# Kernel optimization log

Measured on AMD Instinct MI355X. Metric: run time of the kernel, lower is better.

## Reference

```python
import jax, jax.numpy as jnp
import numpy as np

N = 50000      # nodes
E = 640000     # edges
F_IN = 128
F_OUT = 128


def setup_inputs() -> dict:
    key = jax.random.key(0)
    k1, k2, k3, k4, k5 = jax.random.split(key, 5)
    x = jax.random.normal(k1, (N, F_IN), jnp.float32)
    # binary observation mask (torch: mask.float())
    mask = (jax.random.uniform(k2, (N, F_IN)) < 0.5).astype(jnp.float32)
    edge_index = jax.random.randint(k3, (2, E), 0, N, dtype=jnp.int32)
    W = jax.random.normal(k4, (F_OUT, F_IN), jnp.float32) / np.sqrt(F_IN)
    b = jax.random.normal(k5, (F_OUT,), jnp.float32) * 0.01
    return {"x": x, "mask": mask, "edge_index": edge_index, "W": W, "b": b}


def reference(x, mask, edge_index, W, b):
    row, col = edge_index[0], edge_index[1]

    # --- get_symmetrically_normalized_adjacency: DAD = D^-1/2 A D^-1/2 ---
    ones_e = jnp.ones((edge_index.shape[1],), x.dtype)
    deg = jax.ops.segment_sum(ones_e, col, num_segments=N)
    dinv = jnp.where(deg > 0, deg ** -0.5, 0.0)  # inf -> 0
    w = dinv[row] * dinv[col]                    # [E] normalized edge weights

    def spmm(m):  # (adj @ m)[i] = sum_{e: row_e=i} w_e * m[col_e]
        return jax.ops.segment_sum(w[:, None] * m[col], row, num_segments=N)

    # x[x.isnan()] = 0
    x = jnp.nan_to_num(x)

    # adj @ ones_like(x) == rowsum(adj) broadcast over features
    rowsum = jax.ops.segment_sum(w, row, num_segments=N)  # [N]
    numerator = rowsum[:, None] * spmm(mask * x)          # [N, F_IN]
    denominator = spmm(mask)                              # [N, F_IN]
    ratio = jnp.nan_to_num(numerator / denominator)

    return ratio @ W.T + b
```

## Files before the change

kernel.cpp:

```cpp
#include <hip/hip_runtime.h>
#include <math.h>

#define NN 50000
#define NE 640000
#define F  128
#define NB 196
#define PACKB 12500
#define CHB 256
#define ECHUNK 2500
#define WPAD 136
#define SRCW_N (NE + 8 * NN)

typedef __attribute__((ext_vector_type(8))) short short8;
typedef __attribute__((ext_vector_type(4))) float floatx4;

__device__ inline unsigned f2bf_pk(float f0, float f1) {
    unsigned u0 = __float_as_uint(f0), u1 = __float_as_uint(f1);
    u0 = (u0 + 0x7fffu + ((u0 >> 16) & 1u)) >> 16;
    u1 = (u1 + 0x7fffu + ((u1 >> 16) & 1u)) >> 16;
    return (u1 << 16) | u0;
}

__device__ inline unsigned ilv4(unsigned a, unsigned b) {
    a = (a | (a << 2)) & 0x33u; a = (a | (a << 1)) & 0x55u;
    b = (b | (b << 2)) & 0x33u; b = (b | (b << 1)) & 0x55u;
    return a | (b << 1);
}

__global__ __launch_bounds__(256) void pc_kernel(const float* __restrict__ x,
                                                 const float* __restrict__ mask,
                                                 const int* __restrict__ row,
                                                 const int* __restrict__ col,
                                                 unsigned* __restrict__ mx,
                                                 unsigned char* __restrict__ rec,
                                                 int* __restrict__ crow,
                                                 int* __restrict__ ccol) {
    if (blockIdx.x < PACKB) {
        int lane = threadIdx.x & 63;
        int n = blockIdx.x * 4 + (threadIdx.x >> 6);
        float2 xv = ((const float2*)x)[(size_t)n * 64 + lane];
        float2 mv = ((const float2*)mask)[(size_t)n * 64 + lane];
        float x0 = (xv.x != xv.x) ? 0.f : xv.x;
        float x1 = (xv.y != xv.y) ? 0.f : xv.y;
        float p0 = (mv.x != 0.f) ? x0 : 0.f;
        float p1 = (mv.y != 0.f) ? x1 : 0.f;
        mx[(size_t)n * 64 + lane] = f2bf_pk(p0, p1);
        unsigned long long b0 = __ballot(mv.x != 0.f);
        unsigned long long b1 = __ballot(mv.y != 0.f);
        if (lane < 16) {
            unsigned nib0 = (unsigned)(b0 >> (4 * lane)) & 0xFu;
            unsigned nib1 = (unsigned)(b1 >> (4 * lane)) & 0xFu;
            rec[(size_t)n * 16 + lane] = (unsigned char)ilv4(nib0, nib1);
        }
    } else {
        __shared__ int hr[NB], hc[NB];
        for (int i = threadIdx.x; i < NB; i += 256) { hr[i] = 0; hc[i] = 0; }
        __syncthreads();
        int bid = blockIdx.x - PACKB;
        int e0 = bid * ECHUNK, e1 = e0 + ECHUNK;
        for (int e = e0 + threadIdx.x; e < e1; e += 256) {
            atomicAdd(&hr[row[e] >> 8], 1);
            atomicAdd(&hc[col[e] >> 8], 1);
        }
        __syncthreads();
        for (int i = threadIdx.x; i < NB; i += 256) {
            atomicAdd(&crow[i], hr[i]);
            atomicAdd(&ccol[i], hc[i]);
        }
    }
}

__global__ __launch_bounds__(256) void cscan_kernel(const int* __restrict__ crow,
                                                    const int* __restrict__ ccol,
                                                    int* __restrict__ crow_base,
                                                    int* __restrict__ ccol_base,
                                                    int* __restrict__ crow_cur,
                                                    int* __restrict__ ccol_cur,
                                                    int* __restrict__ rowstart_p) {
    __shared__ int ws[4];
    int t = threadIdx.x, lane = t & 63, wid = t >> 6;
    {
        int v = (t < NB) ? crow[t] : 0;
        int incl = v;
        #pragma unroll
        for (int off = 1; off < 64; off <<= 1) { int s = __shfl_up(incl, off); if (lane >= off) incl += s; }
        if (lane == 63) ws[wid] = incl;
        __syncthreads();
        int wbase = 0;
        for (int k = 0; k < wid; k++) wbase += ws[k];
        int ex = wbase + incl - v;
        if (t < NB) { crow_base[t] = ex; crow_cur[t] = ex; }
        if (t == 0) { crow_base[NB] = NE; rowstart_p[NN] = NE + 8 * NN; }
        __syncthreads();
    }
    {
        int v = (t < NB) ? ccol[t] : 0;
        int incl = v;
        #pragma unroll
        for (int off = 1; off < 64; off <<= 1) { int s = __shfl_up(incl, off); if (lane >= off) incl += s; }
        if (lane == 63) ws[wid] = incl;
        __syncthreads();
        int wbase = 0;
        for (int k = 0; k < wid; k++) wbase += ws[k];
        int ex = wbase + incl - v;
        if (t < NB) { ccol_base[t] = ex; ccol_cur[t] = ex; }
        if (t == 0) ccol_base[NB] = NE;
    }
}

__global__ __launch_bounds__(256) void scatter_kernel(const int* __restrict__ row,
                                                      const int* __restrict__ col,
                                                      int* __restrict__ crow_cur,
                                                      int* __restrict__ ccol_cur,
                                                      unsigned* __restrict__ rrec,
                                                      unsigned char* __restrict__ crec) {
    __shared__ int cntR[NB], cntC[NB], curR[NB], curC[NB];
    for (int i = threadIdx.x; i < NB; i += 256) { cntR[i] = 0; cntC[i] = 0; }
    __syncthreads();
    int e0 = blockIdx.x * ECHUNK, e1 = e0 + ECHUNK;
    for (int e = e0 + threadIdx.x; e < e1; e += 256) {
        atomicAdd(&cntR[row[e] >> 8], 1);
        atomicAdd(&cntC[col[e] >> 8], 1);
    }
    __syncthreads();
    for (int i = threadIdx.x; i < NB; i += 256) {
        curR[i] = atomicAdd(&crow_cur[i], cntR[i]);
        curC[i] = atomicAdd(&ccol_cur[i], cntC[i]);
    }
    __syncthreads();
    for (int e = e0 + threadIdx.x; e < e1; e += 256) {
        int r = row[e], c = col[e];
        int pr = atomicAdd(&curR[r >> 8], 1);
        rrec[pr] = ((unsigned)(r & 255) << 16) | (unsigned)c;
        int pc = atomicAdd(&curC[c >> 8], 1);
        crec[pc] = (unsigned char)(c & 255);
    }
}

__global__ __launch_bounds__(256) void finecol_kernel(const unsigned char* __restrict__ crec,
                                                      const int* __restrict__ ccol_base,
                                                      float* __restrict__ dinv) {
    __shared__ int hist[256];
    int b = blockIdx.x;
    int s0 = ccol_base[b], s1 = ccol_base[b + 1];
    int t = threadIdx.x;
    hist[t] = 0;
    __syncthreads();
    for (int j = s0 + t; j < s1; j += 256)
        atomicAdd(&hist[crec[j]], 1);
    __syncthreads();
    int node = b * 256 + t;
    if (node < NN) {
        int d = hist[t];
        dinv[node] = (d > 0) ? rsqrtf((float)d) : 0.0f;
    }
}

__global__ __launch_bounds__(256) void finerow_kernel(const unsigned* __restrict__ rrec,
                                                      const int* __restrict__ crow_base,
                                                      const float* __restrict__ dinv,
                                                      int* __restrict__ rowstart_p,
                                                      unsigned* __restrict__ srcs_w) {
    __shared__ int hist[256];
    __shared__ int ws[4];
    int b = blockIdx.x;
    int s0 = crow_base[b], s1 = crow_base[b + 1];
    int t = threadIdx.x, lane = t & 63, wid = t >> 6;
    hist[t] = 0;
    __syncthreads();
    for (int j = s0 + t; j < s1; j += 256)
        atomicAdd(&hist[(rrec[j] >> 16) & 255], 1);
    __syncthreads();
    int v = hist[t];
    int incl = v;
    #pragma unroll
    for (int off = 1; off < 64; off <<= 1) { int s = __shfl_up(incl, off); if (lane >= off) incl += s; }
    if (lane == 63) ws[wid] = incl;
    __syncthreads();
    int wbase = 0;
    for (int k = 0; k < wid; k++) wbase += ws[k];
    int ex = wbase + incl - v;
    int pbase = s0 + 2048 * b;
    int node = b * 256 + t;
    if (node < NN) rowstart_p[node] = pbase + ex + 8 * t;
    hist[t] = ex + 8 * t;
    __syncthreads();
    for (int j = s0 + t; j < s1; j += 256) {
        unsigned r2 = rrec[j];
        int c = r2 & 0xFFFF;
        int pos = atomicAdd(&hist[(r2 >> 16) & 255], 1);
        srcs_w[pbase + pos] = f2bf_pk(0.f, dinv[c]) | (unsigned)c;
    }
}

__global__ __launch_bounds__(256) void gather_kernel(
        const int* __restrict__ rowstart_p, const unsigned* __restrict__ srcs_w,
        const float* __restrict__ dinv,
        const uint4* __restrict__ mxv, const unsigned char* __restrict__ rec,
        unsigned* __restrict__ rb) {
    int lane = threadIdx.x & 63;
    int r = blockIdx.x * 4 + (threadIdx.x >> 6);
    int l16 = lane & 15, sub = lane >> 4;
    int s0p = rowstart_p[r];
    int L = rowstart_p[r + 1] - s0p - 8;
    float dr = dinv[r];
    floatx4 n0 = (floatx4)(0.f), n1 = (floatx4)(0.f);
    floatx4 d0 = (floatx4)(0.f), d1 = (floatx4)(0.f);
    float S = 0.f;

    for (int j = 0; j < L; j += 8) {
        #pragma unroll
        for (int g = 0; g < 2; g++) {
            unsigned u = srcs_w[s0p + j + 4 * g + sub];
            int c = u & 0xFFFFu;
            float w = __uint_as_float(u & 0xFFFF0000u);
            uint4 m4 = mxv[c * 16 + l16];
            unsigned mb = rec[c * 16 + l16];
            floatx4 fa, fb;
            fa.x = __uint_as_float(m4.x << 16); fa.y = __uint_as_float(m4.x & 0xffff0000u);
            fa.z = __uint_as_float(m4.y << 16); fa.w = __uint_as_float(m4.y & 0xffff0000u);
            fb.x = __uint_as_float(m4.z << 16); fb.y = __uint_as_float(m4.z & 0xffff0000u);
            fb.z = __uint_as_float(m4.w << 16); fb.w = __uint_as_float(m4.w & 0xffff0000u);
            n0 += w * fa;
            n1 += w * fb;
            d0.x += ((mb >> 0) & 1u) ? w : 0.f;
            d0.y += ((mb >> 1) & 1u) ? w : 0.f;
            d0.z += ((mb >> 2) & 1u) ? w : 0.f;
            d0.w += ((mb >> 3) & 1u) ? w : 0.f;
            d1.x += ((mb >> 4) & 1u) ? w : 0.f;
            d1.y += ((mb >> 5) & 1u) ? w : 0.f;
            d1.z += ((mb >> 6) & 1u) ? w : 0.f;
            d1.w += ((mb >> 7) & 1u) ? w : 0.f;
            S += w;
        }
    }

    float num[8] = {n0.x, n0.y, n0.z, n0.w, n1.x, n1.y, n1.z, n1.w};
    float den[8] = {d0.x, d0.y, d0.z, d0.w, d1.x, d1.y, d1.z, d1.w};
    #pragma unroll
    for (int q = 0; q < 8; q++) {
        num[q] += __shfl_xor(num[q], 16); num[q] += __shfl_xor(num[q], 32);
        den[q] += __shfl_xor(den[q], 16); den[q] += __shfl_xor(den[q], 32);
    }
    S += __shfl_xor(S, 16); S += __shfl_xor(S, 32);

    if (sub == 0) {
        float kf = dr * S;
        float o[8];
        #pragma unroll
        for (int q = 0; q < 8; q++)
            o[q] = (den[q] != 0.f) ? kf * num[q] * __builtin_amdgcn_rcpf(den[q]) : 0.f;
        uint4 pk;
        pk.x = f2bf_pk(o[0], o[1]);
        pk.y = f2bf_pk(o[2], o[3]);
        pk.z = f2bf_pk(o[4], o[5]);
        pk.w = f2bf_pk(o[6], o[7]);
        ((uint4*)rb)[(size_t)r * 16 + l16] = pk;
    }
}

__global__ __launch_bounds__(256) void gemm_kernel(const unsigned short* __restrict__ Ab,
                                                   const float* __restrict__ W,
                                                   const float* __restrict__ bias,
                                                   float* __restrict__ out) {
    __shared__ unsigned short Wlds[F * WPAD];
    int tid = threadIdx.x;

    for (int i = tid * 4; i < F * F; i += 256 * 4) {
        int c = i >> 7, k = i & 127;
        float4 v = *(const float4*)(W + i);
        unsigned lo = f2bf_pk(v.x, v.y);
        unsigned hi = f2bf_pk(v.z, v.w);
        *(uint2*)&Wlds[c * WPAD + k] = make_uint2(lo, hi);
    }
    __syncthreads();

    int lane = tid & 63, wid = tid >> 6;
    int m = lane & 15, quad = lane >> 4;
    int arow = blockIdx.x * 64 + wid * 16 + m;
    int lrow = (arow < NN) ? arow : (NN - 1);
    const unsigned short* Arow = Ab + (size_t)lrow * F + quad * 8;

    floatx4 acc[8];
    #pragma unroll
    for (int nt = 0; nt < 8; nt++) acc[nt] = (floatx4)(0.f);

    #pragma unroll
    for (int step = 0; step < 4; step++) {
        short8 af = *(const short8*)(Arow + step * 32);
        #pragma unroll
        for (int nt = 0; nt < 8; nt++) {
            short8 bf = *(const short8*)&Wlds[(nt * 16 + m) * WPAD + step * 32 + quad * 8];
            acc[nt] = __builtin_amdgcn_mfma_f32_16x16x32_bf16(af, bf, acc[nt], 0, 0, 0);
        }
    }

    int orow0 = blockIdx.x * 64 + wid * 16 + quad * 4;
    #pragma unroll
    for (int nt = 0; nt < 8; nt++) {
        float bv = bias[nt * 16 + m];
        #pragma unroll
        for (int p = 0; p < 4; p++) {
            int gr = orow0 + p;
            if (gr < NN) out[(size_t)gr * F + nt * 16 + m] = acc[nt][p] + bv;
        }
    }
}

extern "C" void kernel_launch(void* const* d_in, const int* in_sizes, int n_in,
                              void* d_out, int out_size, void* d_ws, size_t ws_size,
                              hipStream_t stream) {
    const float* x    = (const float*)d_in[0];
    const float* mask = (const float*)d_in[1];
    const int*   ei   = (const int*)d_in[2];
    const float* W    = (const float*)d_in[3];
    const float* b    = (const float*)d_in[4];
    float* out = (float*)d_out;

    const int* row = ei;
    const int* col = ei + NE;

    unsigned*       mx        = (unsigned*)d_ws;
    unsigned*       rb        = mx + (size_t)NN * 64;
    unsigned*       srcs_w    = rb + (size_t)NN * 64;
    unsigned*       rrec      = srcs_w + SRCW_N;
    unsigned char*  rec       = (unsigned char*)(rrec + NE);
    unsigned char*  crec      = rec + (size_t)NN * 16;
    float*          dinv      = (float*)(crec + NE);
    int*            crow      = (int*)(dinv + NN);
    int*            ccol      = crow + NB;
    int*            crow_base = ccol + NB;
    int*            ccol_base = crow_base + NB + 1;
    int*            crow_cur  = ccol_base + NB + 1;
    int*            ccol_cur  = crow_cur + NB;
    int*            rowstart_p= ccol_cur + NB;

    hipMemsetAsync(crow, 0, 2 * NB * sizeof(int), stream);
    hipMemsetAsync(srcs_w, 0, (size_t)SRCW_N * sizeof(unsigned), stream);

    pc_kernel<<<PACKB + CHB, 256, 0, stream>>>(x, mask, row, col, mx, rec, crow, ccol);
    cscan_kernel<<<1, 256, 0, stream>>>(crow, ccol, crow_base, ccol_base,
                                        crow_cur, ccol_cur, rowstart_p);
    scatter_kernel<<<CHB, 256, 0, stream>>>(row, col, crow_cur, ccol_cur, rrec, crec);
    finecol_kernel<<<NB, 256, 0, stream>>>(crec, ccol_base, dinv);
    finerow_kernel<<<NB, 256, 0, stream>>>(rrec, crow_base, dinv, rowstart_p, srcs_w);
    gather_kernel<<<NN / 4, 256, 0, stream>>>(rowstart_p, srcs_w, dinv,
                                              (const uint4*)mx, rec, rb);
    gemm_kernel<<<(NN + 63) / 64, 256, 0, stream>>>((const unsigned short*)rb, W, b, out);
}
```

Measured before the change: 202.6 us.

## Merge fine row/col kernels, store 16-bit sources and fold dinv into mask records

Merges the degree-histogram and row-bucketing kernels into one launch, so the row side no longer waits for dinv and writes plain 16-bit column indices instead of packed index+weight words. Column dinv now lives inside each node's 32-byte mask record, so the gather reads weight and mask bits from one line. Padding slots point to a zeroed dummy node, which removes the large memset of the source array. It also switches to a true divide in the ratio and nontemporal stores in the GEMM output, at the cost of a slightly larger per-node record.

```diff
diff --git a/kernel.cpp b/kernel.cpp
--- a/kernel.cpp
+++ b/kernel.cpp
@@ -9,7 +9,8 @@
 #define CHB 256
 #define ECHUNK 2500
 #define WPAD 136
-#define SRCW_N (NE + 8 * NN)
+#define RPAD 8
+#define SRCS_N (NE + 256 * RPAD * NB)
 
 typedef __attribute__((ext_vector_type(8))) short short8;
 typedef __attribute__((ext_vector_type(4))) float floatx4;
@@ -50,7 +51,7 @@
         if (lane < 16) {
             unsigned nib0 = (unsigned)(b0 >> (4 * lane)) & 0xFu;
             unsigned nib1 = (unsigned)(b1 >> (4 * lane)) & 0xFu;
-            rec[(size_t)n * 16 + lane] = (unsigned char)ilv4(nib0, nib1);
+            rec[(size_t)n * 32 + lane] = (unsigned char)ilv4(nib0, nib1);
         }
     } else {
         __shared__ int hr[NB], hc[NB];
@@ -76,9 +77,13 @@
                                                     int* __restrict__ ccol_base,
                                                     int* __restrict__ crow_cur,
                                                     int* __restrict__ ccol_cur,
-                                                    int* __restrict__ rowstart_p) {
+                                                    int* __restrict__ rowstart_p,
+                                                    unsigned* __restrict__ mx,
+                                                    unsigned char* __restrict__ rec) {
     __shared__ int ws[4];
     int t = threadIdx.x, lane = t & 63, wid = t >> 6;
+    if (t < 64) mx[(size_t)NN * 64 + t] = 0u;
+    if (t < 8)  ((unsigned*)(rec + (size_t)NN * 32))[t] = 0u;
     {
         int v = (t < NB) ? crow[t] : 0;
         int incl = v;
@@ -90,7 +95,7 @@
         for (int k = 0; k < wid; k++) wbase += ws[k];
         int ex = wbase + incl - v;
         if (t < NB) { crow_base[t] = ex; crow_cur[t] = ex; }
-        if (t == 0) { crow_base[NB] = NE; rowstart_p[NN] = NE + 8 * NN; }
+        if (t == 0) { crow_base[NB] = NE; rowstart_p[NN] = NE + RPAD * NN; }
         __syncthreads();
     }
     {
@@ -137,73 +142,71 @@
     }
 }
 
-__global__ __launch_bounds__(256) void finecol_kernel(const unsigned char* __restrict__ crec,
-                                                      const int* __restrict__ ccol_base,
-                                                      float* __restrict__ dinv) {
-    __shared__ int hist[256];
-    int b = blockIdx.x;
-    int s0 = ccol_base[b], s1 = ccol_base[b + 1];
-    int t = threadIdx.x;
-    hist[t] = 0;
-    __syncthreads();
-    for (int j = s0 + t; j < s1; j += 256)
-        atomicAdd(&hist[crec[j]], 1);
-    __syncthreads();
-    int node = b * 256 + t;
-    if (node < NN) {
-        int d = hist[t];
-        dinv[node] = (d > 0) ? rsqrtf((float)d) : 0.0f;
-    }
-}
-
-__global__ __launch_bounds__(256) void finerow_kernel(const unsigned* __restrict__ rrec,
-                                                      const int* __restrict__ crow_base,
-                                                      const float* __restrict__ dinv,
-                                                      int* __restrict__ rowstart_p,
-                                                      unsigned* __restrict__ srcs_w) {
+__global__ __launch_bounds__(256) void fine_kernel(const unsigned* __restrict__ rrec,
+                                                   const unsigned char* __restrict__ crec,
+                                                   const int* __restrict__ crow_base,
+                                                   const int* __restrict__ ccol_base,
+                                                   int* __restrict__ rowstart_p,
+                                                   unsigned short* __restrict__ srcs,
+                                                   unsigned char* __restrict__ rec) {
     __shared__ int hist[256];
     __shared__ int ws[4];
-    int b = blockIdx.x;
-    int s0 = crow_base[b], s1 = crow_base[b + 1];
     int t = threadIdx.x, lane = t & 63, wid = t >> 6;
     hist[t] = 0;
     __syncthreads();
-    for (int j = s0 + t; j < s1; j += 256)
-        atomicAdd(&hist[(rrec[j] >> 16) & 255], 1);
-    __syncthreads();
-    int v = hist[t];
-    int incl = v;
-    #pragma unroll
-    for (int off = 1; off < 64; off <<= 1) { int s = __shfl_up(incl, off); if (lane >= off) incl += s; }
-    if (lane == 63) ws[wid] = incl;
-    __syncthreads();
-    int wbase = 0;
-    for (int k = 0; k < wid; k++) wbase += ws[k];
-    int ex = wbase + incl - v;
-    int pbase = s0 + 2048 * b;
-    int node = b * 256 + t;
-    if (node < NN) rowstart_p[node] = pbase + ex + 8 * t;
-    hist[t] = ex + 8 * t;
-    __syncthreads();
-    for (int j = s0 + t; j < s1; j += 256) {
-        unsigned r2 = rrec[j];
-        int c = r2 & 0xFFFF;
-        int pos = atomicAdd(&hist[(r2 >> 16) & 255], 1);
-        srcs_w[pbase + pos] = f2bf_pk(0.f, dinv[c]) | (unsigned)c;
+    if (blockIdx.x < NB) {
+        int b = blockIdx.x;
+        int s0 = crow_base[b], s1 = crow_base[b + 1];
+        for (int j = s0 + t; j < s1; j += 256)
+            atomicAdd(&hist[(rrec[j] >> 16) & 255], 1);
+        __syncthreads();
+        int v = hist[t];
+        int incl = v;
+        #pragma unroll
+        for (int off = 1; off < 64; off <<= 1) { int s = __shfl_up(incl, off); if (lane >= off) incl += s; }
+        if (lane == 63) ws[wid] = incl;
+        __syncthreads();
+        int wbase = 0;
+        for (int k = 0; k < wid; k++) wbase += ws[k];
+        int ex = wbase + incl - v;
+        int pbase = s0 + (256 * RPAD) * b;
+        int node = b * 256 + t;
+        int nstart = pbase + ex + RPAD * t;
+        if (node < NN) rowstart_p[node] = nstart;
+        for (int k = 0; k < RPAD; k++)
+            srcs[nstart + v + k] = (unsigned short)NN;
+        hist[t] = ex + RPAD * t;
+        __syncthreads();
+        for (int j = s0 + t; j < s1; j += 256) {
+            unsigned r2 = rrec[j];
+            int pos = atomicAdd(&hist[(r2 >> 16) & 255], 1);
+            srcs[pbase + pos] = (unsigned short)(r2 & 0xFFFFu);
+        }
+    } else {
+        int b = blockIdx.x - NB;
+        int s0 = ccol_base[b], s1 = ccol_base[b + 1];
+        for (int j = s0 + t; j < s1; j += 256)
+            atomicAdd(&hist[crec[j]], 1);
+        __syncthreads();
+        int node = b * 256 + t;
+        if (node < NN) {
+            int d = hist[t];
+            float dv = (d > 0) ? rsqrtf((float)d) : 0.0f;
+            *(float*)(rec + (size_t)node * 32 + 16) = dv;
+        }
     }
 }
 
 __global__ __launch_bounds__(256) void gather_kernel(
-        const int* __restrict__ rowstart_p, const unsigned* __restrict__ srcs_w,
-        const float* __restrict__ dinv,
+        const int* __restrict__ rowstart_p, const unsigned short* __restrict__ srcs,
         const uint4* __restrict__ mxv, const unsigned char* __restrict__ rec,
         unsigned* __restrict__ rb) {
     int lane = threadIdx.x & 63;
     int r = blockIdx.x * 4 + (threadIdx.x >> 6);
     int l16 = lane & 15, sub = lane >> 4;
-    int s0p = rowstart_p[r];
-    int L = rowstart_p[r + 1] - s0p - 8;
-    float dr = dinv[r];
+    int s0 = rowstart_p[r];
+    int L = rowstart_p[r + 1] - s0 - RPAD;
+    float dr = *(const float*)(rec + (size_t)r * 32 + 16);
     floatx4 n0 = (floatx4)(0.f), n1 = (floatx4)(0.f);
     floatx4 d0 = (floatx4)(0.f), d1 = (floatx4)(0.f);
     float S = 0.f;
@@ -211,19 +214,19 @@
     for (int j = 0; j < L; j += 8) {
         #pragma unroll
         for (int g = 0; g < 2; g++) {
-            unsigned u = srcs_w[s0p + j + 4 * g + sub];
-            int c = u & 0xFFFFu;
-            float w = __uint_as_float(u & 0xFFFF0000u);
-            uint4 m4 = mxv[c * 16 + l16];
-            unsigned mb = rec[c * 16 + l16];
+            unsigned c = srcs[s0 + j + 4 * g + sub];
+            unsigned roff = c * 32u;
+            float w = *(const float*)(rec + roff + 16);
+            unsigned mb = rec[roff + l16];
+            uint4 u = mxv[c * 16u + l16];
             floatx4 fa, fb;
-            fa.x = __uint_as_float(m4.x << 16); fa.y = __uint_as_float(m4.x & 0xffff0000u);
-            fa.z = __uint_as_float(m4.y << 16); fa.w = __uint_as_float(m4.y & 0xffff0000u);
-            fb.x = __uint_as_float(m4.z << 16); fb.y = __uint_as_float(m4.z & 0xffff0000u);
-            fb.z = __uint_as_float(m4.w << 16); fb.w = __uint_as_float(m4.w & 0xffff0000u);
+            fa.x = __uint_as_float(u.x << 16); fa.y = __uint_as_float(u.x & 0xffff0000u);
+            fa.z = __uint_as_float(u.y << 16); fa.w = __uint_as_float(u.y & 0xffff0000u);
+            fb.x = __uint_as_float(u.z << 16); fb.y = __uint_as_float(u.z & 0xffff0000u);
+            fb.z = __uint_as_float(u.w << 16); fb.w = __uint_as_float(u.w & 0xffff0000u);
             n0 += w * fa;
             n1 += w * fb;
-            d0.x += ((mb >> 0) & 1u) ? w : 0.f;
+            d0.x += (mb & 1u) ? w : 0.f;
             d0.y += ((mb >> 1) & 1u) ? w : 0.f;
             d0.z += ((mb >> 2) & 1u) ? w : 0.f;
             d0.w += ((mb >> 3) & 1u) ? w : 0.f;
@@ -249,7 +252,7 @@
         float o[8];
         #pragma unroll
         for (int q = 0; q < 8; q++)
-            o[q] = (den[q] != 0.f) ? kf * num[q] * __builtin_amdgcn_rcpf(den[q]) : 0.f;
+            o[q] = (den[q] != 0.f) ? kf * num[q] / den[q] : 0.f;
         uint4 pk;
         pk.x = f2bf_pk(o[0], o[1]);
         pk.y = f2bf_pk(o[2], o[3]);
@@ -302,7 +305,8 @@
         #pragma unroll
         for (int p = 0; p < 4; p++) {
             int gr = orow0 + p;
-            if (gr < NN) out[(size_t)gr * F + nt * 16 + m] = acc[nt][p] + bv;
+            if (gr < NN)
+                __builtin_nontemporal_store(acc[nt][p] + bv, out + (size_t)gr * F + nt * 16 + m);
         }
     }
 }
@@ -321,13 +325,12 @@
     const int* col = ei + NE;
 
     unsigned*       mx        = (unsigned*)d_ws;
-    unsigned*       rb        = mx + (size_t)NN * 64;
-    unsigned*       srcs_w    = rb + (size_t)NN * 64;
-    unsigned*       rrec      = srcs_w + SRCW_N;
-    unsigned char*  rec       = (unsigned char*)(rrec + NE);
-    unsigned char*  crec      = rec + (size_t)NN * 16;
-    float*          dinv      = (float*)(crec + NE);
-    int*            crow      = (int*)(dinv + NN);
+    unsigned*       rb        = mx + (size_t)(NN + 1) * 64;
+    unsigned char*  rec       = (unsigned char*)(rb + (size_t)NN * 64);
+    unsigned*       rrec      = (unsigned*)(rec + (size_t)(NN + 1) * 32);
+    unsigned short* srcs      = (unsigned short*)(rrec + NE);
+    unsigned char*  crec      = (unsigned char*)(srcs + SRCS_N);
+    int*            crow      = (int*)(crec + NE);
     int*            ccol      = crow + NB;
     int*            crow_base = ccol + NB;
     int*            ccol_base = crow_base + NB + 1;
@@ -336,15 +339,14 @@
     int*            rowstart_p= ccol_cur + NB;
 
     hipMemsetAsync(crow, 0, 2 * NB * sizeof(int), stream);
-    hipMemsetAsync(srcs_w, 0, (size_t)SRCW_N * sizeof(unsigned), stream);
 
     pc_kernel<<<PACKB + CHB, 256, 0, stream>>>(x, mask, row, col, mx, rec, crow, ccol);
     cscan_kernel<<<1, 256, 0, stream>>>(crow, ccol, crow_base, ccol_base,
-                                        crow_cur, ccol_cur, rowstart_p);
+                                        crow_cur, ccol_cur, rowstart_p, mx, rec);
     scatter_kernel<<<CHB, 256, 0, stream>>>(row, col, crow_cur, ccol_cur, rrec, crec);
-    finecol_kernel<<<NB, 256, 0, stream>>>(crec, ccol_base, dinv);
-    finerow_kernel<<<NB, 256, 0, stream>>>(rrec, crow_base, dinv, rowstart_p, srcs_w);
-    gather_kernel<<<NN / 4, 256, 0, stream>>>(rowstart_p, srcs_w, dinv,
+    fine_kernel<<<2 * NB, 256, 0, stream>>>(rrec, crec, crow_base, ccol_base,
+                                            rowstart_p, srcs, rec);
+    gather_kernel<<<NN / 4, 256, 0, stream>>>(rowstart_p, srcs,
                                               (const uint4*)mx, rec, rb);
     gemm_kernel<<<(NN + 63) / 64, 256, 0, stream>>>((const unsigned short*)rb, W, b, out);
 }
```

Result: faster. 196.1 us (-3.2%).
